# Kernel tuning notes

Measured on AMD Instinct MI355X. Metric: run time of the kernel, lower is better.

Reference implementation:

```python
import jax, jax.numpy as jnp
import numpy as np

T = 1 << 20          # sequence length
THRESHOLD = 1e-4     # decay-reset threshold (module default)


def setup_inputs() -> dict:
    key = jax.random.key(0)
    X = jax.random.normal(key, (T,), dtype=jnp.float32)
    # stable params near module init [0.2, 0.2, 0.0, 0.0]; small w3/w4 keep the
    # quadratic recurrence bounded while exercising all terms.
    params = jnp.array([0.2, 0.2, 0.05, 0.01], dtype=jnp.float32)
    return {"X": X, "params": params}


def reference(X, params):
    dt = X.dtype
    w1 = jnp.tanh(params[0]); dtanh1 = 1.0 - w1 * w1; d2tanh1 = -2.0 * w1 * dtanh1
    w2 = jnp.tanh(params[1]); dtanh2 = 1.0 - w2 * w2; d2tanh2 = -2.0 * w2 * dtanh2
    w3, w4 = params[2], params[3]

    def step(carry, x):
        h, Jh, Hh, decay = carry  # h:(), Jh:(4,), Hh:(4,4), decay:()
        h_new = w1 * x + w2 * h + w3 * x * x + w4 * h * h
        df_dw = jnp.stack([x * dtanh1, h * dtanh2, x * x, h * h])
        df_dh = w2 + 2.0 * w4 * h
        Jh_new = df_dw + df_dh * Jh
        Hww = (jnp.zeros((4, 4), dt)
               .at[0, 0].set(x * d2tanh1)
               .at[1, 1].set(h * d2tanh2))
        g = jnp.zeros((4,), dt).at[1].set(dtanh2).at[3].set(2.0 * h)
        outer = g[:, None] * Jh[None, :]
        Hh_new = Hww + outer + outer.T + df_dh * Hh
        decay_new = decay * jnp.abs(df_dh)
        reset = decay_new < THRESHOLD
        # torch zero_() mutates storage in-place, so the appended J/H entries at a
        # reset step are also zeroed -> emit post-reset values.
        Jh_out = jnp.where(reset, jnp.zeros((4,), dt), Jh_new)
        Hh_out = jnp.where(reset, jnp.zeros((4, 4), dt), Hh_new)
        h_out = jnp.where(reset, jax.lax.stop_gradient(h_new), h_new)  # detach
        decay_out = jnp.where(reset, jnp.ones((), dt), decay_new)
        return (h_out, Jh_out, Hh_out, decay_out), (h_new, Jh_out, Hh_out)

    init = (jnp.zeros((), dt), jnp.zeros((4,), dt), jnp.zeros((4, 4), dt),
            jnp.ones((), dt))
    _, (hs, Js, Hs) = jax.lax.scan(step, init, X[:-1])
    Z = jnp.concatenate([jnp.zeros((1,), dt), hs])              # [T]
    J = jnp.concatenate([jnp.zeros((1, 4), dt), Js])            # [T, 4]
    H = jnp.concatenate([jnp.zeros((1, 4, 4), dt), Hs])         # [T, 4, 4]
    return Z, J, H
```

## Files before the change

### kernel.cpp

```cpp
#include <hip/hip_runtime.h>
#include <math.h>

#define TLEN (1 << 20)
#define SB 32
#define NSB (TLEN / SB)
#define SCB 256
#define NSCB (NSB / SCB)
#define THRESH 1e-4f
#define IDMAP 0x00FAC688u

#pragma clang fp contract(off)


__global__ void __launch_bounds__(256) k_hscan(const float* __restrict__ P,
                                               const float* __restrict__ X,
                                               float* __restrict__ c,
                                               float* __restrict__ Z) {
#pragma clang fp contract(off)
    __shared__ float sc[4];
    if (threadIdx.x == 0) {
        float w1 = (float)tanh((double)P[0]);
        float w2 = (float)tanh((double)P[1]);
        sc[0] = w1; sc[1] = w2; sc[2] = P[2]; sc[3] = P[3];
        if (blockIdx.x == 0) {
            float dt1 = 1.0f - w1 * w1;
            float dt2 = 1.0f - w2 * w2;
            c[0] = w1; c[1] = w2; c[2] = P[2]; c[3] = P[3];
            c[4] = dt1; c[5] = dt2;
            c[6] = (-2.0f * w1) * dt1; c[7] = (-2.0f * w2) * dt2;
            c[8] = 2.0f * P[3];
        }
    }
    __syncthreads();
    float w1 = sc[0], w2 = sc[1], w3 = sc[2], w4 = sc[3];
    long j = blockIdx.x * (long)blockDim.x + threadIdx.x;
    long o = j * 8;
    if (j >= 3) {
        const float4* xp = (const float4*)(X + o - 24);
        float xa[32];
#pragma unroll
        for (int q = 0; q < 8; ++q) {
            float4 v = xp[q];
            xa[4 * q + 0] = v.x; xa[4 * q + 1] = v.y;
            xa[4 * q + 2] = v.z; xa[4 * q + 3] = v.w;
        }
        float h = 0.0f;
        float out[8];
#pragma unroll
        for (int p = 0; p < 31; ++p) {
            float x = xa[p];
            float t1 = w1 * x;
            float t2 = w2 * h;
            float s1 = t1 + t2;
            float t3 = (w3 * x) * x;
            float s2 = s1 + t3;
            float t4 = (w4 * h) * h;
            h = s2 + t4;
            if (p >= 23) out[p - 23] = h;
        }
        *(float4*)(Z + o) = make_float4(out[0], out[1], out[2], out[3]);
        *(float4*)(Z + o + 4) = make_float4(out[4], out[5], out[6], out[7]);
    } else {
        long b = o - 24; if (b < 0) b = 0;
        long tend = o + 7;
        float h = 0.0f;
        if (o == 0) Z[0] = 0.0f;
        for (long t = b; t < tend; ++t) {
            float x = X[t];
            float t1 = w1 * x;
            float t2 = w2 * h;
            float s1 = t1 + t2;
            float t3 = (w3 * x) * x;
            float s2 = s1 + t3;
            float t4 = (w4 * h) * h;
            h = s2 + t4;
            if (t + 1 >= o) Z[t + 1] = h;
        }
    }
}

__global__ void __launch_bounds__(256) k_tabm(const float* __restrict__ c,
                                              const float* __restrict__ Z,
                                              unsigned int* __restrict__ tab32,
                                              unsigned int* __restrict__ Msk) {
#pragma clang fp contract(off)
    long tid = blockIdx.x * (long)blockDim.x + threadIdx.x;
    if (tid >= (long)NSB * 8) return;
    int i = (int)(tid >> 3);
    int g = (int)(tid & 7);
    float w2 = c[1], w42 = c[8];
    long ci = (long)i * SB;
    long start = ci - g; if (start < 0) start = 0;
    long end = ci + SB;
    float d = 1.0f;
    long last = start;
    unsigned int msk = 0u;
    for (long m = start + 1; m <= end; ++m) {
        float a = w2 + w42 * Z[m - 1];
        d = d * fabsf(a);
        if (d < THRESH) {
            last = m; d = 1.0f;
            if (m > ci) msk |= 1u << (int)(m - ci - 1);
        }
    }
    Msk[(long)i * 8 + g] = msk;
    if (i < NSB - 1) {
        long delta = end - last; if (delta > 7) delta = 7;
        unsigned int v = (unsigned int)delta << (3 * g);
        v |= __shfl_xor(v, 1);
        v |= __shfl_xor(v, 2);
        v |= __shfl_xor(v, 4);
        if (g == 0) tab32[i] = v;
    }
}

__global__ void __launch_bounds__(256) k_scanA(const unsigned int* __restrict__ tab32,
                                               unsigned int* __restrict__ L32,
                                               unsigned int* __restrict__ BT) {
    __shared__ unsigned int buf[2][SCB];
    int t = threadIdx.x;
    long gi = (long)blockIdx.x * SCB + t;
    buf[0][t] = (gi < NSB - 1) ? tab32[gi] : IDMAP;
    __syncthreads();
    int cur = 0;
    for (int off = 1; off < SCB; off <<= 1) {
        unsigned int hi = buf[cur][t];
        unsigned int r;
        if (t >= off) {
            unsigned int lo = buf[cur][t - off];
            r = 0;
#pragma unroll
            for (int g = 0; g < 8; ++g) {
                unsigned int lg = (lo >> (3 * g)) & 7u;
                r |= ((hi >> (3 * lg)) & 7u) << (3 * g);
            }
        } else {
            r = hi;
        }
        buf[cur ^ 1][t] = r;
        __syncthreads();
        cur ^= 1;
    }
    L32[gi] = buf[cur][t];
    if (t == SCB - 1) BT[blockIdx.x] = buf[cur][t];
}

__global__ void __launch_bounds__(256) k_jh7(const float* __restrict__ X,
                                             const float* __restrict__ Z,
                                             const float* __restrict__ c,
                                             const unsigned int* __restrict__ L32,
                                             const unsigned int* __restrict__ BT,
                                             const unsigned int* __restrict__ Msk,
                                             float* __restrict__ Jout,
                                             float* __restrict__ Hout) {
#pragma clang fp contract(off)
    __shared__ unsigned int sBT[NSCB];
    __shared__ unsigned int smsk[64];
    __shared__ unsigned char eL[8];
    __shared__ float zs[264];
    __shared__ float xs[264];
    __shared__ float hx[256 * 17];
    int t = threadIdx.x;
    int B = blockIdx.x;
    float w2 = c[1], dt1 = c[4], dt2 = c[5], d2t1 = c[6], d2t2 = c[7], w42 = c[8];
    long base = (long)B * 256 - 8;
    if (t < NSCB) sBT[t] = BT[t];
    if (t < 16) {
        uint4 v = ((const uint4*)Msk)[(long)B * 16 + t];
        smsk[4 * t] = v.x; smsk[4 * t + 1] = v.y;
        smsk[4 * t + 2] = v.z; smsk[4 * t + 3] = v.w;
    }
    if (t >= 128 && t < 194) {
        int s = t - 128;
        long zi = base + 4l * s;
        float4 v = make_float4(0.f, 0.f, 0.f, 0.f);
        if (zi >= 0) v = *(const float4*)(Z + zi);
        zs[4 * s] = v.x; zs[4 * s + 1] = v.y; zs[4 * s + 2] = v.z; zs[4 * s + 3] = v.w;
    } else if (t >= 194 && t < 256) {
        int s = t - 194;
        long zi = base + 4l * s;
        float4 v = make_float4(0.f, 0.f, 0.f, 0.f);
        if (zi >= 0) v = *(const float4*)(X + zi);
        xs[4 * s] = v.x; xs[4 * s + 1] = v.y; xs[4 * s + 2] = v.z; xs[4 * s + 3] = v.w;
    } else if (t >= 64 && t < 68) {
        int s = t - 64 + 62;
        long zi = base + 4l * s;
        float4 v = make_float4(0.f, 0.f, 0.f, 0.f);
        if (zi >= 0) v = *(const float4*)(X + zi);
        xs[4 * s] = v.x; xs[4 * s + 1] = v.y; xs[4 * s + 2] = v.z; xs[4 * s + 3] = v.w;
    }
    __syncthreads();
    if (t < 8) {
        int i = B * 8 + t;
        int e = 0;
        if (i > 0) {
            int bp = (i - 1) >> 8;
            unsigned int g = 0;
            for (int k = 0; k < bp; ++k) g = (sBT[k] >> (3 * g)) & 7u;
            e = (int)((L32[i - 1] >> (3 * g)) & 7u);
        }
        eL[t] = (unsigned char)e;
    }
    __syncthreads();
    long q = (long)B * 256 + t;
    int il = t >> 5;
    int j = t & 31;
    int e = (int)eL[il];
    unsigned int mask = smsk[il * 8 + e];
    unsigned int bits = mask & ((j > 0) ? ((1u << j) - 1u) : 0u);
    int a = bits ? (j + __clz(bits) - 32) : (j + e);

    float J0 = 0, J1 = 0, J2 = 0, J3 = 0;
    float H00 = 0, H01 = 0, H03 = 0, H11 = 0, H12 = 0, H13 = 0, H23 = 0, H33 = 0;
    if (a > 0) {
        long m0 = q - a + 1;
        {
            int ix = (int)(m0 - 1 - base);
            float x = xs[ix];
            float h = zs[ix];
            H00 = x * d2t1; H11 = h * d2t2;
            J0 = x * dt1; J1 = h * dt2; J2 = x * x; J3 = h * h;
        }
        for (long m = m0 + 1; m <= q; ++m) {
            int ix = (int)(m - 1 - base);
            float x = xs[ix];
            float h = zs[ix];
            float av = w2 + w42 * h;
            float g3 = 2.0f * h;
            float g1J0 = dt2 * J0, g1J1 = dt2 * J1, g1J2 = dt2 * J2, g1J3 = dt2 * J3;
            float g3J0 = g3 * J0, g3J1 = g3 * J1, g3J2 = g3 * J2, g3J3 = g3 * J3;
            float n00 = (x * d2t1) + av * H00;
            float n01 = g1J0 + av * H01;
            float n03 = g3J0 + av * H03;
            float n11 = (((h * d2t2) + g1J1) + g1J1) + av * H11;
            float n12 = g1J2 + av * H12;
            float n13 = (g1J3 + g3J1) + av * H13;
            float n23 = g3J2 + av * H23;
            float n33 = (g3J3 + g3J3) + av * H33;
            H00 = n00; H01 = n01; H03 = n03; H11 = n11;
            H12 = n12; H13 = n13; H23 = n23; H33 = n33;
            J0 = (x * dt1) + av * J0;
            J1 = (h * dt2) + av * J1;
            J2 = (x * x) + av * J2;
            J3 = (h * h) + av * J3;
        }
    }
    *((float4*)(Jout + 4 * q)) = make_float4(J0, J1, J2, J3);
    float* hr = hx + t * 17;
    hr[0]  = H00; hr[1]  = H01; hr[2]  = 0.0f; hr[3]  = H03;
    hr[4]  = H01; hr[5]  = H11; hr[6]  = H12;  hr[7]  = H13;
    hr[8]  = 0.0f; hr[9] = H12; hr[10] = 0.0f; hr[11] = H23;
    hr[12] = H03; hr[13] = H13; hr[14] = H23;  hr[15] = H33;
    __syncthreads();
    float4* Hp = (float4*)Hout + (long)B * 1024;
#pragma unroll
    for (int rr = 0; rr < 4; ++rr) {
        int f = 256 * rr + t;
        int o = f >> 2;
        int cc = (f & 3) * 4;
        const float* s = hx + o * 17 + cc;
        Hp[f] = make_float4(s[0], s[1], s[2], s[3]);
    }
}

extern "C" void kernel_launch(void* const* d_in, const int* in_sizes, int n_in,
                              void* d_out, int out_size, void* d_ws, size_t ws_size,
                              hipStream_t stream) {
    const float* X = (const float*)d_in[0];
    const float* P = (const float*)d_in[1];
    float* out = (float*)d_out;
    float* Z = out;
    float* Jout = out + (long)TLEN;
    float* Hout = out + 5l * TLEN;

    char* ws = (char*)d_ws;
    float* consts = (float*)ws;
    unsigned int* BT = (unsigned int*)(ws + 64);
    unsigned int* tab32 = (unsigned int*)(ws + 1024);
    unsigned int* L32 = (unsigned int*)(ws + 1024 + (size_t)NSB * 4);
    unsigned int* Msk = (unsigned int*)(ws + 1024 + 2 * (size_t)NSB * 4);

    hipLaunchKernelGGL(k_hscan, dim3(TLEN / 8 / 256), dim3(256), 0, stream,
                       P, X, consts, Z);
    hipLaunchKernelGGL(k_tabm, dim3(NSB * 8 / 256), dim3(256), 0, stream,
                       consts, Z, tab32, Msk);
    hipLaunchKernelGGL(k_scanA, dim3(NSCB), dim3(SCB), 0, stream,
                       tab32, L32, BT);
    hipLaunchKernelGGL(k_jh7, dim3(TLEN / 256), dim3(256), 0, stream,
                       X, Z, consts, L32, BT, Msk, Jout, Hout);
}
```

Baseline: 40.23 us.

## Fuse decay-table computation into block scan with LDS-staged Z window

Merges the per-chunk decay/reset table kernel into the block-level composition scan, removing one launch and the tab32 round trip through global memory. Each block stages its Z window into padded LDS with float4 loads. Each thread then computes all 8 offset variants in registers, sharing one |w2+2w4 h| evaluation across them. The cost is fewer threads doing the table work: 32K threads instead of 256K, each with longer serial loops, which may reduce parallelism.

```diff
diff --git a/kernel.cpp b/kernel.cpp
--- a/kernel.cpp
+++ b/kernel.cpp
@@ -8,6 +8,10 @@
 #define NSCB (NSB / SCB)
 #define THRESH 1e-4f
 #define IDMAP 0x00FAC688u
+
+#define WWORDS (SCB * SB + 8)
+#define WPAD(i) ((i) + ((i) >> 5))
+#define LDSW WPAD(WWORDS)
 
 #pragma clang fp contract(off)
 
@@ -79,48 +83,85 @@
     }
 }
 
-__global__ void __launch_bounds__(256) k_tabm(const float* __restrict__ c,
-                                              const float* __restrict__ Z,
-                                              unsigned int* __restrict__ tab32,
-                                              unsigned int* __restrict__ Msk) {
+__global__ void __launch_bounds__(256) k_tabscan(const float* __restrict__ c,
+                                                 const float* __restrict__ Z,
+                                                 unsigned int* __restrict__ L32,
+                                                 unsigned int* __restrict__ BT,
+                                                 unsigned int* __restrict__ Msk) {
 #pragma clang fp contract(off)
-    long tid = blockIdx.x * (long)blockDim.x + threadIdx.x;
-    if (tid >= (long)NSB * 8) return;
-    int i = (int)(tid >> 3);
-    int g = (int)(tid & 7);
-    float w2 = c[1], w42 = c[8];
-    long ci = (long)i * SB;
-    long start = ci - g; if (start < 0) start = 0;
-    long end = ci + SB;
-    float d = 1.0f;
-    long last = start;
-    unsigned int msk = 0u;
-    for (long m = start + 1; m <= end; ++m) {
-        float a = w2 + w42 * Z[m - 1];
-        d = d * fabsf(a);
-        if (d < THRESH) {
-            last = m; d = 1.0f;
-            if (m > ci) msk |= 1u << (int)(m - ci - 1);
-        }
-    }
-    Msk[(long)i * 8 + g] = msk;
-    if (i < NSB - 1) {
-        long delta = end - last; if (delta > 7) delta = 7;
-        unsigned int v = (unsigned int)delta << (3 * g);
-        v |= __shfl_xor(v, 1);
-        v |= __shfl_xor(v, 2);
-        v |= __shfl_xor(v, 4);
-        if (g == 0) tab32[i] = v;
-    }
-}
-
-__global__ void __launch_bounds__(256) k_scanA(const unsigned int* __restrict__ tab32,
-                                               unsigned int* __restrict__ L32,
-                                               unsigned int* __restrict__ BT) {
+    __shared__ float zw[LDSW];
     __shared__ unsigned int buf[2][SCB];
     int t = threadIdx.x;
-    long gi = (long)blockIdx.x * SCB + t;
-    buf[0][t] = (gi < NSB - 1) ? tab32[gi] : IDMAP;
+    int b = blockIdx.x;
+    long wo = (long)b * (SCB * SB) - 8;
+    for (int v = 0; v < 9; ++v) {
+        int q = v * 256 + t;
+        if (q < WWORDS / 4) {
+            long zi = wo + 4l * q;
+            float4 val = make_float4(0.f, 0.f, 0.f, 0.f);
+            if (zi >= 0) val = *(const float4*)(Z + zi);
+            int r0 = 4 * q;
+            zw[WPAD(r0 + 0)] = val.x;
+            zw[WPAD(r0 + 1)] = val.y;
+            zw[WPAD(r0 + 2)] = val.z;
+            zw[WPAD(r0 + 3)] = val.w;
+        }
+    }
+    __syncthreads();
+    float w2 = c[1], w42 = c[8];
+    long gi = (long)b * SCB + t;
+    int rbase = t * 32 + 8;
+    unsigned int m32;
+    unsigned int msk[8];
+    {
+        float d[8]; int last[8];
+#pragma unroll
+        for (int g = 0; g < 8; ++g) { d[g] = 1.0f; last[g] = -g; msk[g] = 0u; }
+        if (gi == 0) {
+#pragma unroll
+            for (int g = 0; g < 8; ++g) last[g] = 0;
+            for (int k = 0; k < 32; ++k) {
+                float fa = fabsf(w2 + w42 * zw[WPAD(rbase + k)]);
+#pragma unroll
+                for (int g = 0; g < 8; ++g) {
+                    d[g] = d[g] * fa;
+                    if (d[g] < THRESH) { last[g] = k + 1; d[g] = 1.0f; msk[g] |= 1u << k; }
+                }
+            }
+        } else {
+#pragma unroll
+            for (int p = 0; p < 7; ++p) {
+                float fa = fabsf(w2 + w42 * zw[WPAD(rbase + p - 7)]);
+#pragma unroll
+                for (int g = 7 - p; g < 8; ++g) {
+                    d[g] = d[g] * fa;
+                    if (d[g] < THRESH) { last[g] = p - 6; d[g] = 1.0f; }
+                }
+            }
+            for (int k = 0; k < 32; ++k) {
+                float fa = fabsf(w2 + w42 * zw[WPAD(rbase + k)]);
+#pragma unroll
+                for (int g = 0; g < 8; ++g) {
+                    d[g] = d[g] * fa;
+                    if (d[g] < THRESH) { last[g] = k + 1; d[g] = 1.0f; msk[g] |= 1u << k; }
+                }
+            }
+        }
+        if (gi < NSB - 1) {
+            m32 = 0;
+#pragma unroll
+            for (int g = 0; g < 8; ++g) {
+                int delta = 32 - last[g]; if (delta > 7) delta = 7;
+                m32 |= (unsigned int)delta << (3 * g);
+            }
+        } else {
+            m32 = IDMAP;
+        }
+    }
+    uint4* mp = (uint4*)Msk + gi * 2;
+    mp[0] = make_uint4(msk[0], msk[1], msk[2], msk[3]);
+    mp[1] = make_uint4(msk[4], msk[5], msk[6], msk[7]);
+    buf[0][t] = m32;
     __syncthreads();
     int cur = 0;
     for (int off = 1; off < SCB; off <<= 1) {
@@ -142,7 +183,7 @@
         cur ^= 1;
     }
     L32[gi] = buf[cur][t];
-    if (t == SCB - 1) BT[blockIdx.x] = buf[cur][t];
+    if (t == SCB - 1) BT[b] = buf[cur][t];
 }
 
 __global__ void __launch_bounds__(256) k_jh7(const float* __restrict__ X,
@@ -276,16 +317,13 @@
     char* ws = (char*)d_ws;
     float* consts = (float*)ws;
     unsigned int* BT = (unsigned int*)(ws + 64);
-    unsigned int* tab32 = (unsigned int*)(ws + 1024);
-    unsigned int* L32 = (unsigned int*)(ws + 1024 + (size_t)NSB * 4);
-    unsigned int* Msk = (unsigned int*)(ws + 1024 + 2 * (size_t)NSB * 4);
+    unsigned int* L32 = (unsigned int*)(ws + 1024);
+    unsigned int* Msk = (unsigned int*)(ws + 1024 + (size_t)NSB * 4);
 
     hipLaunchKernelGGL(k_hscan, dim3(TLEN / 8 / 256), dim3(256), 0, stream,
                        P, X, consts, Z);
-    hipLaunchKernelGGL(k_tabm, dim3(NSB * 8 / 256), dim3(256), 0, stream,
-                       consts, Z, tab32, Msk);
-    hipLaunchKernelGGL(k_scanA, dim3(NSCB), dim3(SCB), 0, stream,
-                       tab32, L32, BT);
+    hipLaunchKernelGGL(k_tabscan, dim3(NSCB), dim3(SCB), 0, stream,
+                       consts, Z, L32, BT, Msk);
     hipLaunchKernelGGL(k_jh7, dim3(TLEN / 256), dim3(256), 0, stream,
                        X, Z, consts, L32, BT, Msk, Jout, Hout);
 }
```

Result: slower. 43.30 us (+7.6%).
